# Optimization experiments

Hardware: AMD Instinct MI355X
Metric: run time of the kernel (lower is better)

## Reference

```python
import jax, jax.numpy as jnp
import numpy as np

B, S, D = 2, 2048, 1024
N_HEAD, D_ATTN = 16, 64


def setup_inputs() -> dict:
    key = jax.random.key(0)
    ks = jax.random.split(key, 5)
    x = jax.random.normal(ks[0], (B, S, D), dtype=jnp.float32)
    # causal mask: True = masked (as consumed by torch.masked_fill)
    mask = jnp.triu(jnp.ones((S, S), dtype=bool), k=1)
    scale = 0.02
    w_q = jax.random.normal(ks[1], (D, N_HEAD * D_ATTN), dtype=jnp.float32) * scale
    w_k = jax.random.normal(ks[2], (D, N_HEAD * D_ATTN), dtype=jnp.float32) * scale
    w_v = jax.random.normal(ks[3], (D, N_HEAD * D_ATTN), dtype=jnp.float32) * scale
    w_o = jax.random.normal(ks[4], (N_HEAD * D_ATTN, D), dtype=jnp.float32) * scale
    return {"x": x, "mask": mask, "w_q": w_q, "w_k": w_k, "w_v": w_v, "w_o": w_o}


def _split(t):
    # [B,S,H*Da] -> [B,H,S,Da]
    b, s, _ = t.shape
    return t.reshape(b, s, N_HEAD, D_ATTN).transpose(0, 2, 1, 3)


def reference(x, mask, w_q, w_k, w_v, w_o):
    q = _split(x @ w_q)
    k = _split(x @ w_k)
    v = _split(x @ w_v)
    scale = D_ATTN ** 0.5
    score = jnp.einsum("bhqd,bhkd->bhqk", q, k) / scale  # [B,H,S,S]
    score = jnp.where(mask, -jnp.inf, score)
    prob = jax.nn.softmax(score, axis=-1)
    out = jnp.einsum("bhqk,bhkd->bhqd", prob, v)
    out = out.transpose(0, 2, 1, 3).reshape(x.shape[0], x.shape[1], N_HEAD * D_ATTN)
    return out @ w_o
```

## Files before the change

### kernel.cpp

```cpp
#include <hip/hip_runtime.h>
#include <stdint.h>

using u16 = unsigned short;
using u32 = unsigned int;
using u64 = unsigned long long;

typedef float f32x4 __attribute__((ext_vector_type(4)));
typedef __bf16 bf16x8 __attribute__((ext_vector_type(8)));

#define DEV static __device__ __forceinline__

DEV u16 f2bf(float f) {
  u32 u = __float_as_uint(f);
  u += 0x7FFFu + ((u >> 16) & 1u);
  return (u16)(u >> 16);
}

DEV void gld16(const void* g, void* l) {
  __builtin_amdgcn_global_load_lds((__attribute__((address_space(1))) void*)g,
                                   (__attribute__((address_space(3))) void*)l,
                                   16, 0, 0);
}

__global__ void k_cvt(const float* __restrict__ x, u16* __restrict__ xb,
                      const float* __restrict__ w0, const float* __restrict__ w1,
                      const float* __restrict__ w2, const float* __restrict__ w3,
                      u16* __restrict__ t0, u16* __restrict__ t1,
                      u16* __restrict__ t2, u16* __restrict__ t3) {
  const int tid = threadIdx.x;
  if (blockIdx.x < 2048) {
    int i = (blockIdx.x * 256 + tid) * 8;
    float4 a = *(const float4*)&x[i];
    float4 b = *(const float4*)&x[i + 4];
    __align__(16) u16 o[8];
    o[0] = f2bf(a.x); o[1] = f2bf(a.y); o[2] = f2bf(a.z); o[3] = f2bf(a.w);
    o[4] = f2bf(b.x); o[5] = f2bf(b.y); o[6] = f2bf(b.z); o[7] = f2bf(b.w);
    *(uint4*)&xb[i] = *(const uint4*)o;
    return;
  }
  const int c = blockIdx.x - 2048;
  const int z = c >> 8, rem = c & 255;
  const float* w = z == 0 ? w0 : z == 1 ? w1 : z == 2 ? w2 : w3;
  u16* wt       = z == 0 ? t0 : z == 1 ? t1 : z == 2 ? t2 : t3;
  __shared__ __align__(16) float tile[64][68];
  const int k0 = (rem & 15) * 64, n0 = (rem >> 4) * 64;
#pragma unroll
  for (int i = 0; i < 4; ++i) {
    int cc = tid + i * 256;
    int kr = cc >> 4, col = (cc & 15) * 4;
    *(float4*)&tile[kr][col] = *(const float4*)&w[(size_t)(k0 + kr) * 1024 + n0 + col];
  }
  __syncthreads();
#pragma unroll
  for (int i = 0; i < 2; ++i) {
    int cc = tid + i * 256;
    int nr = cc >> 3, kc = (cc & 7) * 8;
    __align__(16) u16 o[8];
#pragma unroll
    for (int j = 0; j < 8; ++j) o[j] = f2bf(tile[kc + j][nr]);
    *(uint4*)&wt[(size_t)(n0 + nr) * 1024 + k0 + kc] = *(const uint4*)o;
  }
}

DEV void gemm8_mainloop(const u16* __restrict__ A, const u16* __restrict__ Bt,
                        int m0, int n0, u16* Asb, u16* Bsb, f32x4 (&acc)[4][2]) {
  const int tid = threadIdx.x;
  const int lane = tid & 63;
  const int lo = lane & 15, hi = lane >> 4;
  const int wv = tid >> 6;
  const int wm = (wv >> 2) * 64, wn = (wv & 3) * 32;

#pragma unroll
  for (int f = 0; f < 4; ++f)
#pragma unroll
    for (int g = 0; g < 2; ++g) {
      f32x4 z = {0.f, 0.f, 0.f, 0.f};
      acc[f][g] = z;
    }

  const int r = tid >> 2;
  const int bblk = (tid & 3) ^ (r & 3) ^ ((r >> 2) & 3);
  const u16* ga = A + (size_t)(m0 + r) * 1024 + bblk * 8;
  const u16* gb = Bt + (size_t)(n0 + r) * 1024 + bblk * 8;
  const int dst = wv * 512;

  int aoff[4], boff[2];
#pragma unroll
  for (int f = 0; f < 4; ++f) {
    int ra = wm + f * 16 + lo;
    aoff[f] = ra * 32 + ((hi ^ (ra & 3) ^ ((ra >> 2) & 3)) * 8);
  }
#pragma unroll
  for (int g = 0; g < 2; ++g) {
    int rb = wn + g * 16 + lo;
    boff[g] = rb * 32 + ((hi ^ (rb & 3) ^ ((rb >> 2) & 3)) * 8);
  }

#pragma unroll
  for (int p = 0; p < 2; ++p) {
    const int k0 = p * 32, bo = p * 4096;
    gld16(ga + k0, Asb + bo + dst);
    gld16(gb + k0, Bsb + bo + dst);
  }

#pragma unroll 1
  for (int kt = 0; kt < 32; ++kt) {
    if (kt < 31) asm volatile("s_waitcnt vmcnt(2)" ::: "memory");
    else         asm volatile("s_waitcnt vmcnt(0)" ::: "memory");
    __builtin_amdgcn_s_barrier();
    __builtin_amdgcn_sched_barrier(0);

    if (kt + 2 < 32) {
      const int k0 = (kt + 2) * 32, bo = ((kt + 2) % 3) * 4096;
      gld16(ga + k0, Asb + bo + dst);
      gld16(gb + k0, Bsb + bo + dst);
    }

    const int bo = (kt % 3) * 4096;
    bf16x8 af[4], bf[2];
#pragma unroll
    for (int f = 0; f < 4; ++f) af[f] = *(const bf16x8*)&Asb[bo + aoff[f]];
#pragma unroll
    for (int g = 0; g < 2; ++g) bf[g] = *(const bf16x8*)&Bsb[bo + boff[g]];
#pragma unroll
    for (int f = 0; f < 4; ++f)
#pragma unroll
      for (int g = 0; g < 2; ++g)
        acc[f][g] = __builtin_amdgcn_mfma_f32_16x16x32_bf16(af[f], bf[g], acc[f][g], 0, 0, 0);
  }
}

__global__ __launch_bounds__(512, 6) void k_gemm_qkv(
    const u16* __restrict__ X, const u16* __restrict__ Wq, const u16* __restrict__ Wk,
    const u16* __restrict__ Wv, u16* __restrict__ Q, u16* __restrict__ K,
    u16* __restrict__ Vt) {
  __shared__ __align__(16) u16 SH[24576];
  u16* Asb = SH;
  u16* Bsb = SH + 12288;
  const int nb = blockIdx.x, mb = blockIdx.y;
  const int proj = nb >> 3, n0 = (nb & 7) * 128;
  const u16* W = proj == 0 ? Wq : proj == 1 ? Wk : Wv;
  const float scl = proj == 0 ? 0.125f * 1.4426950408889634f : 1.0f;
  f32x4 acc[4][2];
  gemm8_mainloop(X, W, mb * 128, n0, Asb, Bsb, acc);

  const int tid = threadIdx.x;
  const int lane = tid & 63, wv = tid >> 6;
  const int lo = lane & 15, hi = lane >> 4;
  const int wm = (wv >> 2) * 64, wn = (wv & 3) * 32;
  const int b = (mb * 128) >> 11;
  const int sbase = (mb * 128) & 2047;
  const int h0 = n0 >> 6;

  __syncthreads();

  if (proj == 2) {
    u16 (*Ctv)[132] = (u16(*)[132])SH;
#pragma unroll
    for (int f = 0; f < 4; ++f)
#pragma unroll
      for (int g = 0; g < 2; ++g)
#pragma unroll
        for (int rr = 0; rr < 4; ++rr)
          Ctv[wn + g * 16 + lo][wm + f * 16 + hi * 4 + rr] = f2bf(acc[f][g][rr]);
    __syncthreads();
    const int g2 = tid & 15;
    const int bp = ((g2 >> 2) & 1) * 32 + ((g2 >> 1) & 1) * 16 + (g2 & 1) * 8 +
                   ((g2 >> 3) & 1) * 4;
#pragma unroll
    for (int p = 0; p < 8; ++p) {
      const int ci = p * 32 + (tid >> 4);
      const int blk = ci & 1, d = (ci >> 1) & 63, hl = ci >> 7;
      u64 v = *(const u64*)&Ctv[hl * 64 + d][blk * 64 + g2 * 4];
      *(u64*)&Vt[((size_t)((b * 16 + h0 + hl) * 64 + d)) * 2048 +
                 sbase + blk * 64 + bp] = v;
    }
  } else {
    u16* Dst = proj == 0 ? Q : K;
    u16 (*Ct)[132] = (u16(*)[132])SH;
#pragma unroll
    for (int f = 0; f < 4; ++f)
#pragma unroll
      for (int g = 0; g < 2; ++g)
#pragma unroll
        for (int rr = 0; rr < 4; ++rr)
          Ct[wm + f * 16 + hi * 4 + rr][wn + g * 16 + lo] = f2bf(acc[f][g][rr] * scl);
    __syncthreads();
#pragma unroll
    for (int p = 0; p < 4; ++p) {
      const int row = p * 32 + (tid >> 4);
      const int ch = tid & 15;
      const int h = h0 + (ch >> 3), d = (ch & 7) * 8;
      __align__(16) u16 o[8];
#pragma unroll
      for (int q = 0; q < 8; ++q) o[q] = Ct[row][ch * 8 + q];
      *(uint4*)&Dst[(size_t)((b * 16 + h) * 2048 + sbase + row) * 64 + d] = *(const uint4*)o;
    }
  }
}

__global__ __launch_bounds__(512, 2) void k_gemm_out(
    const u16* __restrict__ A, const u16* __restrict__ Wt, float* __restrict__ Out) {
  __shared__ __align__(16) u16 Asb[3 * 4096];
  __shared__ __align__(16) u16 Bsb[3 * 4096];
  const int nb = blockIdx.x, mb = blockIdx.y;
  f32x4 acc[4][2];
  gemm8_mainloop(A, Wt, mb * 128, nb * 128, Asb, Bsb, acc);
  const int lane = threadIdx.x & 63, wv = threadIdx.x >> 6;
  const int lo = lane & 15, hi = lane >> 4;
  const int wm = (wv >> 2) * 64, wn = (wv & 3) * 32;
#pragma unroll
  for (int f = 0; f < 4; ++f)
#pragma unroll
    for (int g = 0; g < 2; ++g)
#pragma unroll
      for (int rr = 0; rr < 4; ++rr) {
        int m = mb * 128 + wm + f * 16 + hi * 4 + rr;
        int n = nb * 128 + wn + g * 16 + lo;
        Out[(size_t)m * 1024 + n] = acc[f][g][rr];
      }
}

DEV void qk_tile(const u16* Kc, const bf16x8 (&qf)[2], int lo, int hi, f32x4 (&sc)[4]) {
#pragma unroll
  for (int cf = 0; cf < 4; ++cf) {
    f32x4 z = {0.f, 0.f, 0.f, 0.f};
    sc[cf] = z;
#pragma unroll
    for (int kf = 0; kf < 2; ++kf) {
      int row = cf * 16 + lo;
      int blk = ((kf * 4 + hi) ^ (row & 7)) * 8;
      bf16x8 kfr = *(const bf16x8*)&Kc[row * 64 + blk];
      sc[cf] = __builtin_amdgcn_mfma_f32_16x16x32_bf16(kfr, qf[kf], sc[cf], 0, 0, 0);
    }
  }
}

DEV void sm_pv(f32x4 (&sc)[4], const u16* Vc, int lane, int lo, int hi,
               float& m_run, float& l_run, f32x4 (&ao)[4]) {
  bf16x8 vfr[4][2];
#pragma unroll
  for (int df = 0; df < 4; ++df)
#pragma unroll
    for (int kf = 0; kf < 2; ++kf) {
      int row = df * 16 + lo;
      int blk = ((kf * 4 + hi) ^ (row & 7)) * 8;
      vfr[df][kf] = *(const bf16x8*)&Vc[row * 64 + blk];
    }

  float mx0 = fmaxf(fmaxf(sc[0][0], sc[0][1]), fmaxf(sc[0][2], sc[0][3]));
  float mx1 = fmaxf(fmaxf(sc[1][0], sc[1][1]), fmaxf(sc[1][2], sc[1][3]));
  float mx2 = fmaxf(fmaxf(sc[2][0], sc[2][1]), fmaxf(sc[2][2], sc[2][3]));
  float mx3 = fmaxf(fmaxf(sc[3][0], sc[3][1]), fmaxf(sc[3][2], sc[3][3]));
  float mx = fmaxf(fmaxf(mx0, mx1), fmaxf(mx2, mx3));
  mx = fmaxf(mx, __shfl_xor(mx, 16));
  mx = fmaxf(mx, __shfl_xor(mx, 32));

  if (__any(mx > m_run + 8.0f)) {
    float mnew = fmaxf(m_run, mx);
    float sclf = __builtin_amdgcn_exp2f(m_run - mnew);
    const int base = lane & 48;
#pragma unroll
    for (int r = 0; r < 4; ++r) {
      float s_r = __shfl(sclf, base + hi * 4 + r);
#pragma unroll
      for (int df = 0; df < 4; ++df) ao[df][r] *= s_r;
    }
    l_run *= sclf;
    m_run = mnew;
  }

  float pp[4];
  bf16x8 pa0, pa1;
#pragma unroll
  for (int cf = 0; cf < 4; ++cf) {
    float p0 = __builtin_amdgcn_exp2f(sc[cf][0] - m_run);
    float p1 = __builtin_amdgcn_exp2f(sc[cf][1] - m_run);
    float p2 = __builtin_amdgcn_exp2f(sc[cf][2] - m_run);
    float p3 = __builtin_amdgcn_exp2f(sc[cf][3] - m_run);
    pp[cf] = (p0 + p1) + (p2 + p3);
    bf16x8& pa = (cf & 1) ? pa1 : pa0;
    int j = (cf >> 1) * 4;
    pa[j] = (__bf16)p0; pa[j + 1] = (__bf16)p1;
    pa[j + 2] = (__bf16)p2; pa[j + 3] = (__bf16)p3;
  }
  l_run += (pp[0] + pp[1]) + (pp[2] + pp[3]);

  __builtin_amdgcn_s_setprio(1);
#pragma unroll
  for (int df = 0; df < 4; ++df) {
#pragma unroll
    for (int kf = 0; kf < 2; ++kf)
      ao[df] = __builtin_amdgcn_mfma_f32_16x16x32_bf16(kf == 0 ? pa0 : pa1, vfr[df][kf],
                                                       ao[df], 0, 0, 0);
  }
  __builtin_amdgcn_s_setprio(0);
}

__global__ __launch_bounds__(512) void k_attn(
    const u16* __restrict__ Qg, const u16* __restrict__ Kg,
    const u16* __restrict__ Vtg, u16* __restrict__ Og) {
  __shared__ __align__(16) u16 Ks[4][64 * 64];
  __shared__ __align__(16) u16 Vs[4][64 * 64];
  const int tid = threadIdx.x, lane = tid & 63, wv = tid >> 6;
  const int lo = lane & 15, hi = lane >> 4;
  const int w4 = wv & 3, qsel = wv >> 2;

  const int flat = blockIdx.y * 16 + blockIdx.x;
  const int xcd = flat & 7, slot = flat >> 3;
  const int q4 = slot >> 4, rsl = slot & 15;
  const int bh = xcd * 4 + q4;
  const int jp = (q4 & 2) ? (15 - rsl) : rsl;

  const u16* Qb = Qg + (size_t)bh * 2048 * 64;
  const u16* Kb = Kg + (size_t)bh * 2048 * 64;
  const u16* Vb = Vtg + (size_t)bh * 64 * 2048;
  const int b = bh >> 4, h = bh & 15;

  const int nta = jp + 1, ntb = 32 - jp;
  const int q0 = (qsel ? (31 - jp) : jp) * 64;
  const int myNt = qsel ? ntb : nta;
  const int qq = q0 + w4 * 16 + lo;

  bf16x8 qf[2];
#pragma unroll
  for (int kf = 0; kf < 2; ++kf)
    qf[kf] = *(const bf16x8*)&Qb[(size_t)(q0 + w4 * 16 + lo) * 64 + kf * 32 + hi * 8];

  f32x4 ao[4];
#pragma unroll
  for (int df = 0; df < 4; ++df) {
    f32x4 z = {0.f, 0.f, 0.f, 0.f};
    ao[df] = z;
  }
  float m_run = -1e30f, l_run = 0.f;

  const int r0 = tid >> 3;
  const int e0 = ((tid & 7) ^ (r0 & 7)) * 8;

#pragma unroll
  for (int p = 0; p < 3; ++p) {
    gld16(Kb + (size_t)(p * 64 + r0) * 64 + e0, &Ks[p][wv * 512]);
    gld16(Vb + (size_t)r0 * 2048 + p * 64 + e0, &Vs[p][wv * 512]);
  }

#pragma unroll 1
  for (int t = 0; t < ntb; ++t) {
    if (t + 2 < ntb)      asm volatile("s_waitcnt vmcnt(4)" ::: "memory");
    else if (t + 1 < ntb) asm volatile("s_waitcnt vmcnt(2)" ::: "memory");
    else                  asm volatile("s_waitcnt vmcnt(0)" ::: "memory");
    __builtin_amdgcn_s_barrier();
    __builtin_amdgcn_sched_barrier(0);

    if (t + 3 < ntb) {
      const int kn = (t + 3) * 64;
      gld16(Kb + (size_t)(kn + r0) * 64 + e0, &Ks[(t + 3) & 3][wv * 512]);
      gld16(Vb + (size_t)r0 * 2048 + kn + e0, &Vs[(t + 3) & 3][wv * 512]);
    }

    if (t < myNt) {
      const u16* Kc = Ks[t & 3];
      const u16* Vc = Vs[t & 3];
      f32x4 sc[4];
      __builtin_amdgcn_s_setprio(1);
      qk_tile(Kc, qf, lo, hi, sc);
      __builtin_amdgcn_s_setprio(0);

      if (t == myNt - 1) {
        const int kv0 = t * 64;
#pragma unroll
        for (int cf = 0; cf < 4; ++cf)
#pragma unroll
          for (int r = 0; r < 4; ++r) {
            int kk = kv0 + cf * 16 + hi * 4 + r;
            if (kk > qq) sc[cf][r] = -1e30f;
          }
      }

      sm_pv(sc, Vc, lane, lo, hi, m_run, l_run, ao);
    }
  }

  float l_tot = l_run;
  l_tot += __shfl_xor(l_tot, 16);
  l_tot += __shfl_xor(l_tot, 32);
  float linv[4];
  const int base = lane & 48;
#pragma unroll
  for (int r = 0; r < 4; ++r) {
    float l_r = __shfl(l_tot, base + hi * 4 + r);
    linv[r] = 1.0f / l_r;
  }
#pragma unroll
  for (int df = 0; df < 4; ++df)
#pragma unroll
    for (int r = 0; r < 4; ++r) {
      int s = q0 + w4 * 16 + hi * 4 + r;
      int d = df * 16 + lo;
      Og[((size_t)(b * 2048 + s)) * 1024 + h * 64 + d] = f2bf(ao[df][r] * linv[r]);
    }
}

extern "C" void kernel_launch(void* const* d_in, const int* in_sizes, int n_in,
                              void* d_out, int out_size, void* d_ws, size_t ws_size,
                              hipStream_t stream) {
  const float* x = (const float*)d_in[0];
  const float* wq = (const float*)d_in[2];
  const float* wk = (const float*)d_in[3];
  const float* wv = (const float*)d_in[4];
  const float* wo = (const float*)d_in[5];

  char* ws = (char*)d_ws;
  u16* xb  = (u16*)(ws);
  u16* wqt = (u16*)(ws + 8388608);
  u16* wkt = (u16*)(ws + 8388608 + 2097152);
  u16* wvt = (u16*)(ws + 8388608 + 2 * 2097152);
  u16* wot = (u16*)(ws + 8388608 + 3 * 2097152);
  u16* qb  = (u16*)(ws + 16777216);
  u16* kb  = (u16*)(ws + 16777216 + 8388608);
  u16* vt  = (u16*)(ws + 16777216 + 3 * 8388608);
  u16* ao  = (u16*)(ws + 16777216 + 4 * 8388608);

  k_cvt<<<dim3(3072), dim3(256), 0, stream>>>(x, xb, wq, wk, wv, wo, wqt, wkt, wvt, wot);
  k_gemm_qkv<<<dim3(24, 32), dim3(512), 0, stream>>>(xb, wqt, wkt, wvt, qb, kb, vt);
  k_attn<<<dim3(16, 32), dim3(512), 0, stream>>>(qb, kb, vt, ao);
  k_gemm_out<<<dim3(8, 32), dim3(512), 0, stream>>>(ao, wot, (float*)d_out);
}
```

Baseline: 109.4 us.

## Switch QKV GEMM to 32x32x16 MFMA with 4-wave 64x64 warp tiles

Adds a new mainloop for the QKV projection GEMM that uses 32x32x16 bf16 MFMA instructions. The block shrinks from 8 to 4 waves, and each wave now computes a 64x64 sub-tile instead of 64x32, loading two LDS chunks per thread per stage. The aim is more reuse of each LDS fragment per MFMA and fewer LDS reads per flop. The epilogue is remapped to the 32x32 accumulator layout, and launch bounds change to 256 threads with 3 blocks per CU. Each wave holds more accumulator registers, and latency hiding with fewer waves is a risk.

```diff
diff --git a/kernel.cpp b/kernel.cpp
--- a/kernel.cpp
+++ b/kernel.cpp
@@ -6,6 +6,7 @@
 using u64 = unsigned long long;
 
 typedef float f32x4 __attribute__((ext_vector_type(4)));
+typedef float f32x16 __attribute__((ext_vector_type(16)));
 typedef __bf16 bf16x8 __attribute__((ext_vector_type(8)));
 
 #define DEV static __device__ __forceinline__
@@ -62,75 +63,88 @@
   }
 }
 
-DEV void gemm8_mainloop(const u16* __restrict__ A, const u16* __restrict__ Bt,
-                        int m0, int n0, u16* Asb, u16* Bsb, f32x4 (&acc)[4][2]) {
+DEV void gemm32_mainloop(const u16* __restrict__ A, const u16* __restrict__ Bt,
+                         int m0, int n0, u16* Asb, u16* Bsb, f32x16 (&acc)[2][2]) {
   const int tid = threadIdx.x;
   const int lane = tid & 63;
-  const int lo = lane & 15, hi = lane >> 4;
+  const int lo31 = lane & 31, g2 = lane >> 5;
   const int wv = tid >> 6;
-  const int wm = (wv >> 2) * 64, wn = (wv & 3) * 32;
-
-#pragma unroll
-  for (int f = 0; f < 4; ++f)
-#pragma unroll
-    for (int g = 0; g < 2; ++g) {
-      f32x4 z = {0.f, 0.f, 0.f, 0.f};
-      acc[f][g] = z;
-    }
-
-  const int r = tid >> 2;
-  const int bblk = (tid & 3) ^ (r & 3) ^ ((r >> 2) & 3);
-  const u16* ga = A + (size_t)(m0 + r) * 1024 + bblk * 8;
-  const u16* gb = Bt + (size_t)(n0 + r) * 1024 + bblk * 8;
-  const int dst = wv * 512;
-
-  int aoff[4], boff[2];
-#pragma unroll
-  for (int f = 0; f < 4; ++f) {
-    int ra = wm + f * 16 + lo;
-    aoff[f] = ra * 32 + ((hi ^ (ra & 3) ^ ((ra >> 2) & 3)) * 8);
-  }
-#pragma unroll
-  for (int g = 0; g < 2; ++g) {
-    int rb = wn + g * 16 + lo;
-    boff[g] = rb * 32 + ((hi ^ (rb & 3) ^ ((rb >> 2) & 3)) * 8);
-  }
+  const int wm = (wv >> 1) * 64, wn = (wv & 1) * 64;
+
+#pragma unroll
+  for (int fi = 0; fi < 2; ++fi)
+#pragma unroll
+    for (int gj = 0; gj < 2; ++gj)
+#pragma unroll
+      for (int e = 0; e < 16; ++e) acc[fi][gj][e] = 0.f;
+
+  const int c0 = tid, c1 = tid + 256;
+  const int r0 = c0 >> 2, r1 = c1 >> 2;
+  const int b0 = (c0 & 3) ^ (r0 & 3) ^ ((r0 >> 2) & 3);
+  const int b1 = (c1 & 3) ^ (r1 & 3) ^ ((r1 >> 2) & 3);
+  const u16* ga0 = A + (size_t)(m0 + r0) * 1024 + b0 * 8;
+  const u16* ga1 = A + (size_t)(m0 + r1) * 1024 + b1 * 8;
+  const u16* gb0 = Bt + (size_t)(n0 + r0) * 1024 + b0 * 8;
+  const u16* gb1 = Bt + (size_t)(n0 + r1) * 1024 + b1 * 8;
+  const int da0 = wv * 512, da1 = wv * 512 + 2048;
+
+  int aoff[2][2], boff[2][2];
+#pragma unroll
+  for (int fi = 0; fi < 2; ++fi)
+#pragma unroll
+    for (int ks = 0; ks < 2; ++ks) {
+      int ra = wm + fi * 32 + lo31;
+      aoff[fi][ks] = ra * 32 + (((ks * 2 + g2) ^ (ra & 3) ^ ((ra >> 2) & 3)) * 8);
+      int rb = wn + fi * 32 + lo31;
+      boff[fi][ks] = rb * 32 + (((ks * 2 + g2) ^ (rb & 3) ^ ((rb >> 2) & 3)) * 8);
+    }
 
 #pragma unroll
   for (int p = 0; p < 2; ++p) {
     const int k0 = p * 32, bo = p * 4096;
-    gld16(ga + k0, Asb + bo + dst);
-    gld16(gb + k0, Bsb + bo + dst);
+    gld16(ga0 + k0, Asb + bo + da0);
+    gld16(ga1 + k0, Asb + bo + da1);
+    gld16(gb0 + k0, Bsb + bo + da0);
+    gld16(gb1 + k0, Bsb + bo + da1);
   }
 
 #pragma unroll 1
   for (int kt = 0; kt < 32; ++kt) {
-    if (kt < 31) asm volatile("s_waitcnt vmcnt(2)" ::: "memory");
+    if (kt < 31) asm volatile("s_waitcnt vmcnt(4)" ::: "memory");
     else         asm volatile("s_waitcnt vmcnt(0)" ::: "memory");
     __builtin_amdgcn_s_barrier();
     __builtin_amdgcn_sched_barrier(0);
 
     if (kt + 2 < 32) {
       const int k0 = (kt + 2) * 32, bo = ((kt + 2) % 3) * 4096;
-      gld16(ga + k0, Asb + bo + dst);
-      gld16(gb + k0, Bsb + bo + dst);
+      gld16(ga0 + k0, Asb + bo + da0);
+      gld16(ga1 + k0, Asb + bo + da1);
+      gld16(gb0 + k0, Bsb + bo + da0);
+      gld16(gb1 + k0, Bsb + bo + da1);
     }
 
     const int bo = (kt % 3) * 4096;
-    bf16x8 af[4], bf[2];
-#pragma unroll
-    for (int f = 0; f < 4; ++f) af[f] = *(const bf16x8*)&Asb[bo + aoff[f]];
-#pragma unroll
-    for (int g = 0; g < 2; ++g) bf[g] = *(const bf16x8*)&Bsb[bo + boff[g]];
-#pragma unroll
-    for (int f = 0; f < 4; ++f)
-#pragma unroll
-      for (int g = 0; g < 2; ++g)
-        acc[f][g] = __builtin_amdgcn_mfma_f32_16x16x32_bf16(af[f], bf[g], acc[f][g], 0, 0, 0);
-  }
-}
-
-__global__ __launch_bounds__(512, 6) void k_gemm_qkv(
+    bf16x8 af[2][2], bfv[2][2];
+#pragma unroll
+    for (int fi = 0; fi < 2; ++fi)
+#pragma unroll
+      for (int ks = 0; ks < 2; ++ks) {
+        af[fi][ks]  = *(const bf16x8*)&Asb[bo + aoff[fi][ks]];
+        bfv[fi][ks] = *(const bf16x8*)&Bsb[bo + boff[fi][ks]];
+      }
+#pragma unroll
+    for (int fi = 0; fi < 2; ++fi)
+#pragma unroll
+      for (int gj = 0; gj < 2; ++gj) {
+        acc[fi][gj] = __builtin_amdgcn_mfma_f32_32x32x16_bf16(af[fi][0], bfv[gj][0],
+                                                              acc[fi][gj], 0, 0, 0);
+        acc[fi][gj] = __builtin_amdgcn_mfma_f32_32x32x16_bf16(af[fi][1], bfv[gj][1],
+                                                              acc[fi][gj], 0, 0, 0);
+      }
+  }
+}
+
+__global__ __launch_bounds__(256, 3) void k_gemm_qkv(
     const u16* __restrict__ X, const u16* __restrict__ Wq, const u16* __restrict__ Wk,
     const u16* __restrict__ Wv, u16* __restrict__ Q, u16* __restrict__ K,
     u16* __restrict__ Vt) {
@@ -141,13 +155,13 @@
   const int proj = nb >> 3, n0 = (nb & 7) * 128;
   const u16* W = proj == 0 ? Wq : proj == 1 ? Wk : Wv;
   const float scl = proj == 0 ? 0.125f * 1.4426950408889634f : 1.0f;
-  f32x4 acc[4][2];
-  gemm8_mainloop(X, W, mb * 128, n0, Asb, Bsb, acc);
+  f32x16 acc[2][2];
+  gemm32_mainloop(X, W, mb * 128, n0, Asb, Bsb, acc);
 
   const int tid = threadIdx.x;
   const int lane = tid & 63, wv = tid >> 6;
-  const int lo = lane & 15, hi = lane >> 4;
-  const int wm = (wv >> 2) * 64, wn = (wv & 3) * 32;
+  const int lo31 = lane & 31, g2 = lane >> 5;
+  const int wm = (wv >> 1) * 64, wn = (wv & 1) * 64;
   const int b = (mb * 128) >> 11;
   const int sbase = (mb * 128) & 2047;
   const int h0 = n0 >> 6;
@@ -157,21 +171,24 @@
   if (proj == 2) {
     u16 (*Ctv)[132] = (u16(*)[132])SH;
 #pragma unroll
-    for (int f = 0; f < 4; ++f)
-#pragma unroll
-      for (int g = 0; g < 2; ++g)
-#pragma unroll
-        for (int rr = 0; rr < 4; ++rr)
-          Ctv[wn + g * 16 + lo][wm + f * 16 + hi * 4 + rr] = f2bf(acc[f][g][rr]);
+    for (int fi = 0; fi < 2; ++fi)
+#pragma unroll
+      for (int gj = 0; gj < 2; ++gj)
+#pragma unroll
+        for (int e = 0; e < 16; ++e) {
+          int ml = wm + fi * 32 + (e & 3) + 8 * (e >> 2) + 4 * g2;
+          int nl = wn + gj * 32 + lo31;
+          Ctv[nl][ml] = f2bf(acc[fi][gj][e]);
+        }
     __syncthreads();
-    const int g2 = tid & 15;
-    const int bp = ((g2 >> 2) & 1) * 32 + ((g2 >> 1) & 1) * 16 + (g2 & 1) * 8 +
-                   ((g2 >> 3) & 1) * 4;
-#pragma unroll
-    for (int p = 0; p < 8; ++p) {
-      const int ci = p * 32 + (tid >> 4);
+    const int gidx = tid & 15;
+    const int bp = ((gidx >> 2) & 1) * 32 + ((gidx >> 1) & 1) * 16 + (gidx & 1) * 8 +
+                   ((gidx >> 3) & 1) * 4;
+#pragma unroll
+    for (int p = 0; p < 16; ++p) {
+      const int ci = p * 16 + (tid >> 4);
       const int blk = ci & 1, d = (ci >> 1) & 63, hl = ci >> 7;
-      u64 v = *(const u64*)&Ctv[hl * 64 + d][blk * 64 + g2 * 4];
+      u64 v = *(const u64*)&Ctv[hl * 64 + d][blk * 64 + gidx * 4];
       *(u64*)&Vt[((size_t)((b * 16 + h0 + hl) * 64 + d)) * 2048 +
                  sbase + blk * 64 + bp] = v;
     }
@@ -179,16 +196,19 @@
     u16* Dst = proj == 0 ? Q : K;
     u16 (*Ct)[132] = (u16(*)[132])SH;
 #pragma unroll
-    for (int f = 0; f < 4; ++f)
-#pragma unroll
-      for (int g = 0; g < 2; ++g)
-#pragma unroll
-        for (int rr = 0; rr < 4; ++rr)
-          Ct[wm + f * 16 + hi * 4 + rr][wn + g * 16 + lo] = f2bf(acc[f][g][rr] * scl);
+    for (int fi = 0; fi < 2; ++fi)
+#pragma unroll
+      for (int gj = 0; gj < 2; ++gj)
+#pragma unroll
+        for (int e = 0; e < 16; ++e) {
+          int ml = wm + fi * 32 + (e & 3) + 8 * (e >> 2) + 4 * g2;
+          int nl = wn + gj * 32 + lo31;
+          Ct[ml][nl] = f2bf(acc[fi][gj][e] * scl);
+        }
     __syncthreads();
 #pragma unroll
-    for (int p = 0; p < 4; ++p) {
-      const int row = p * 32 + (tid >> 4);
+    for (int p = 0; p < 8; ++p) {
+      const int row = p * 16 + (tid >> 4);
       const int ch = tid & 15;
       const int h = h0 + (ch >> 3), d = (ch & 7) * 8;
       __align__(16) u16 o[8];
@@ -196,6 +216,74 @@
       for (int q = 0; q < 8; ++q) o[q] = Ct[row][ch * 8 + q];
       *(uint4*)&Dst[(size_t)((b * 16 + h) * 2048 + sbase + row) * 64 + d] = *(const uint4*)o;
     }
+  }
+}
+
+DEV void gemm8_mainloop(const u16* __restrict__ A, const u16* __restrict__ Bt,
+                        int m0, int n0, u16* Asb, u16* Bsb, f32x4 (&acc)[4][2]) {
+  const int tid = threadIdx.x;
+  const int lane = tid & 63;
+  const int lo = lane & 15, hi = lane >> 4;
+  const int wv = tid >> 6;
+  const int wm = (wv >> 2) * 64, wn = (wv & 3) * 32;
+
+#pragma unroll
+  for (int f = 0; f < 4; ++f)
+#pragma unroll
+    for (int g = 0; g < 2; ++g) {
+      f32x4 z = {0.f, 0.f, 0.f, 0.f};
+      acc[f][g] = z;
+    }
+
+  const int r = tid >> 2;
+  const int bblk = (tid & 3) ^ (r & 3) ^ ((r >> 2) & 3);
+  const u16* ga = A + (size_t)(m0 + r) * 1024 + bblk * 8;
+  const u16* gb = Bt + (size_t)(n0 + r) * 1024 + bblk * 8;
+  const int dst = wv * 512;
+
+  int aoff[4], boff[2];
+#pragma unroll
+  for (int f = 0; f < 4; ++f) {
+    int ra = wm + f * 16 + lo;
+    aoff[f] = ra * 32 + ((hi ^ (ra & 3) ^ ((ra >> 2) & 3)) * 8);
+  }
+#pragma unroll
+  for (int g = 0; g < 2; ++g) {
+    int rb = wn + g * 16 + lo;
+    boff[g] = rb * 32 + ((hi ^ (rb & 3) ^ ((rb >> 2) & 3)) * 8);
+  }
+
+#pragma unroll
+  for (int p = 0; p < 2; ++p) {
+    const int k0 = p * 32, bo = p * 4096;
+    gld16(ga + k0, Asb + bo + dst);
+    gld16(gb + k0, Bsb + bo + dst);
+  }
+
+#pragma unroll 1
+  for (int kt = 0; kt < 32; ++kt) {
+    if (kt < 31) asm volatile("s_waitcnt vmcnt(2)" ::: "memory");
+    else         asm volatile("s_waitcnt vmcnt(0)" ::: "memory");
+    __builtin_amdgcn_s_barrier();
+    __builtin_amdgcn_sched_barrier(0);
+
+    if (kt + 2 < 32) {
+      const int k0 = (kt + 2) * 32, bo = ((kt + 2) % 3) * 4096;
+      gld16(ga + k0, Asb + bo + dst);
+      gld16(gb + k0, Bsb + bo + dst);
+    }
+
+    const int bo = (kt % 3) * 4096;
+    bf16x8 af[4], bf[2];
+#pragma unroll
+    for (int f = 0; f < 4; ++f) af[f] = *(const bf16x8*)&Asb[bo + aoff[f]];
+#pragma unroll
+    for (int g = 0; g < 2; ++g) bf[g] = *(const bf16x8*)&Bsb[bo + boff[g]];
+#pragma unroll
+    for (int f = 0; f < 4; ++f)
+#pragma unroll
+      for (int g = 0; g < 2; ++g)
+        acc[f][g] = __builtin_amdgcn_mfma_f32_16x16x32_bf16(af[f], bf[g], acc[f][g], 0, 0, 0);
   }
 }
 
@@ -422,7 +510,7 @@
   u16* ao  = (u16*)(ws + 16777216 + 4 * 8388608);
 
   k_cvt<<<dim3(3072), dim3(256), 0, stream>>>(x, xb, wq, wk, wv, wo, wqt, wkt, wvt, wot);
-  k_gemm_qkv<<<dim3(24, 32), dim3(512), 0, stream>>>(xb, wqt, wkt, wvt, qb, kb, vt);
+  k_gemm_qkv<<<dim3(24, 32), dim3(256), 0, stream>>>(xb, wqt, wkt, wvt, qb, kb, vt);
   k_attn<<<dim3(16, 32), dim3(512), 0, stream>>>(qb, kb, vt, ao);
   k_gemm_out<<<dim3(8, 32), dim3(512), 0, stream>>>(ao, wot, (float*)d_out);
 }
```

Measured after the change: 110.3 us. About the same (+0.8%).
